# Kernel optimization log

Measured on AMD Instinct MI355X. Metric: run time of the kernel, lower is better.

## Reference

```python
import jax, jax.numpy as jnp
import numpy as np
import math

DEPTH = 3
NUM_GRAPHS = 8
BN_EPS = 1e-5
POOL_RATIO = 0.5


def _gcn(A, x, W, b):
    # GCNConv(improved=True): A_hat = A + 2*I; out = D^-1/2 A_hat D^-1/2 (x W) + b
    n = A.shape[0]
    A_hat = A + 2.0 * jnp.eye(n, dtype=A.dtype)
    deg = A_hat.sum(axis=1)
    d = jnp.where(deg > 0, jax.lax.rsqrt(deg), 0.0)
    return d[:, None] * (A_hat @ (d[:, None] * (x @ W))) + b


def _bn_eval(x, g, b):
    # BatchNorm1d in eval mode with running_mean=0, running_var=1
    return x * (g / jnp.sqrt(1.0 + BN_EPS)) + b


def _forward(x, edge_index, batch, conv0_w, conv0_b, down_w, down_b, pool_w,
             up_w, up_b, lins_w, lins_b, bn_g, bn_b, out_w, out_b):
    n0 = x.shape[0]
    # dense weighted adjacency A[dst, src] += 1 (duplicates sum, same as scatter-add MP)
    A = jnp.zeros((n0, n0), x.dtype).at[edge_index[1], edge_index[0]].add(1.0)

    # ---- GraphUNet (eval mode: dropout p=0.92 is identity) ----
    h = jax.nn.relu(_gcn(A, x, conv0_w, conv0_b))
    xs, As, perms = [h], [A], []
    for i in range(DEPTH):
        n = A.shape[0]
        eye = jnp.eye(n, dtype=A.dtype)
        S = A + eye                       # add_self_loops(weight=1)
        A2 = (S @ S) * (1.0 - eye)        # spspmm then remove_self_loops
        # TopKPooling: score = tanh((x.w)/||w||), keep top ceil(0.5*n) nodes
        score = jnp.tanh((h @ pool_w[i]) / jnp.linalg.norm(pool_w[i]))
        k = math.ceil(POOL_RATIO * n)
        _, perm = jax.lax.top_k(score, k)
        h = h[perm] * score[perm][:, None]
        A = A2[perm][:, perm]             # filter_adj
        h = jax.nn.relu(_gcn(A, h, down_w[i], down_b[i]))
        if i < DEPTH - 1:
            xs.append(h)
            As.append(A)
        perms.append(perm)
    for i in range(DEPTH):
        j = DEPTH - 1 - i
        res, Aj, perm = xs[j], As[j], perms[j]
        up = jnp.zeros_like(res).at[perm].set(h)
        h = res + up                      # sum_res=True skip connection
        h = _gcn(Aj, h, up_w[i], up_b[i])
        if i < DEPTH - 1:
            h = jax.nn.relu(h)

    # ---- global_add_pool + BN/Linear/tanh head ----
    g = jax.ops.segment_sum(h, batch, num_segments=NUM_GRAPHS)
    for i in range(3):
        g = _bn_eval(g, bn_g[i], bn_b[i])
        g = jnp.tanh(g @ lins_w[i] + lins_b[i])
    g = _bn_eval(g, bn_g[3], bn_b[3])
    return g @ out_w + out_b


def setup_inputs() -> dict:
    key = jax.random.key(0)
    ks = jax.random.split(key, 20)
    N, F, H, O, E = 4096, 64, 128, 32, 65536
    s = 0.05
    x = jax.random.normal(ks[0], (N, F), jnp.float32)
    src = jax.random.randint(ks[1], (E,), 0, N)
    dst = jax.random.randint(ks[2], (E,), 0, N)
    edge_index = jnp.stack([jnp.concatenate([src, dst]),
                            jnp.concatenate([dst, src])]).astype(jnp.int32)
    batch = jnp.sort(jax.random.randint(ks[3], (N,), 0, NUM_GRAPHS)).astype(jnp.int32)
    return {
        "x": x,
        "edge_index": edge_index,
        "batch": batch,
        "conv0_w": jax.random.normal(ks[4], (F, H), jnp.float32) * s,
        "conv0_b": jnp.zeros((H,), jnp.float32),
        "down_w": jax.random.normal(ks[5], (DEPTH, H, H), jnp.float32) * s,
        "down_b": jnp.zeros((DEPTH, H), jnp.float32),
        "pool_w": jax.random.normal(ks[6], (DEPTH, H), jnp.float32),
        "up_w": jax.random.normal(ks[7], (DEPTH, H, H), jnp.float32) * s,
        "up_b": jnp.zeros((DEPTH, H), jnp.float32),
        "lins_w": jax.random.normal(ks[8], (3, H, H), jnp.float32) * s,
        "lins_b": jnp.zeros((3, H), jnp.float32),
        "bn_g": jnp.ones((4, H), jnp.float32),
        "bn_b": jnp.zeros((4, H), jnp.float32),
        "out_w": jax.random.normal(ks[9], (H, O), jnp.float32) * s,
        "out_b": jnp.zeros((O,), jnp.float32),
    }


def reference(x, edge_index, batch, conv0_w, conv0_b, down_w, down_b, pool_w,
              up_w, up_b, lins_w, lins_b, bn_g, bn_b, out_w, out_b):
    return _forward(x, edge_index, batch, conv0_w, conv0_b, down_w, down_b,
                    pool_w, up_w, up_b, lins_w, lins_b, bn_g, bn_b, out_w, out_b)
```

## Files before the change

kernel.cpp:

```cpp
#include <hip/hip_runtime.h>
#include <math.h>

#define H 128
#define NG 8

typedef __attribute__((ext_vector_type(8))) short bf16x8;
typedef __attribute__((ext_vector_type(8))) unsigned short ushort8;
typedef __attribute__((ext_vector_type(4))) float f32x4;

static __device__ __forceinline__ float b2f(unsigned short u) {
  union { unsigned int i; float f; } v;
  v.i = ((unsigned int)u) << 16;
  return v.f;
}
static __device__ __forceinline__ unsigned short f2b(float f) {
  return (unsigned short)(__float_as_uint(f) >> 16);
}

__global__ void k_hist(const int* __restrict__ ei, int E, int* __restrict__ cnt) {
  int e = blockIdx.x * 256 + threadIdx.x;
  if (e >= E) return;
  atomicAdd(&cnt[ei[E + e]], 1);
}

__global__ __launch_bounds__(1024) void k_scan(const int* __restrict__ cnt,
                                               int* __restrict__ rowptr, int n) {
  __shared__ int sums[1024];
  int tid = threadIdx.x;
  int base = tid * 4;
  int v0 = 0, v1 = 0, v2 = 0, v3 = 0;
  if (base < n) { v0 = cnt[base]; v1 = cnt[base + 1]; v2 = cnt[base + 2]; v3 = cnt[base + 3]; }
  int s = v0 + v1 + v2 + v3;
  sums[tid] = s;
  __syncthreads();
  for (int off = 1; off < 1024; off <<= 1) {
    int t = (tid >= off) ? sums[tid - off] : 0;
    __syncthreads();
    sums[tid] += t;
    __syncthreads();
  }
  int excl = sums[tid] - s;
  if (base < n) {
    rowptr[base] = excl;
    rowptr[base + 1] = excl + v0;
    rowptr[base + 2] = excl + v0 + v1;
    rowptr[base + 3] = excl + v0 + v1 + v2;
  }
  if (tid == 1023) rowptr[n] = sums[1023];
}

__global__ void k_fill(const int* __restrict__ ei, int E, const int* __restrict__ rowptr,
                       int* __restrict__ cursor, int* __restrict__ colidx) {
  int e = blockIdx.x * 256 + threadIdx.x;
  if (e >= E) return;
  int r = ei[E + e], c = ei[e];
  int p = atomicAdd(&cursor[r], 1);
  colidx[rowptr[r] + p] = c;
}

__global__ void k_dvcnt(const int* __restrict__ cnt, float* __restrict__ dv, int n) {
  int i = blockIdx.x * 256 + threadIdx.x;
  if (i < n) dv[i] = rsqrtf((float)cnt[i] + 2.0f);
}

__global__ void k_deg(const float* __restrict__ A, int n, float* __restrict__ dv) {
  int row = blockIdx.x * (blockDim.x >> 6) + (threadIdx.x >> 6);
  int lane = threadIdx.x & 63;
  if (row >= n) return;
  float s = 0.f;
  const float* arow = A + (size_t)row * n;
  for (int j = lane; j < n; j += 64) s += arow[j];
#pragma unroll
  for (int o = 32; o > 0; o >>= 1) s += __shfl_down(s, o);
  if (lane == 0) dv[row] = rsqrtf(s + 2.0f);
}

template <int MODE>
__global__ __launch_bounds__(256) void k_xw(const float* __restrict__ X,
                                            const float* __restrict__ W,
                                            const float* __restrict__ dv,
                                            const int* __restrict__ idx,
                                            const float* __restrict__ aux,
                                            float* __restrict__ Y, int n, int F) {
  __shared__ float Xs[64][36];
  __shared__ float Ws[32][132];
  __shared__ int ridx[64];
  __shared__ float rscl[64];
  int tid = threadIdx.x;
  int rowBase = blockIdx.x * 64;
  if (MODE == 1) {
    if (tid < 64) {
      int pp = idx[rowBase + tid];
      ridx[tid] = pp;
      rscl[tid] = aux[pp];
    }
  } else if (MODE == 2) {
    if (tid < 64) ridx[tid] = idx[rowBase + tid];
  }
  if (MODE != 0) __syncthreads();
  int r0 = (tid >> 5) << 3;
  int c0 = (tid & 31) << 2;
  float acc[8][4] = {};
  for (int k0 = 0; k0 < F; k0 += 32) {
#pragma unroll
    for (int it = 0, e = tid; it < 8; ++it, e += 256) {
      int ii = e >> 5, kk = e & 31;
      int gk = k0 + kk;
      float v;
      if (MODE == 0) {
        v = X[(size_t)(rowBase + ii) * F + gk];
      } else if (MODE == 1) {
        v = X[(size_t)ridx[ii] * F + gk] * rscl[ii];
      } else {
        v = X[(size_t)(rowBase + ii) * F + gk];
        int iv = ridx[ii];
        if (iv >= 0) v += aux[(size_t)iv * H + gk];
      }
      Xs[ii][kk] = v;
    }
#pragma unroll
    for (int it = 0, e = tid; it < 4; ++it, e += 256) {
      int kk = e >> 5, cc4 = e & 31;
      *(float4*)&Ws[kk][cc4 << 2] = *(const float4*)&W[(size_t)(k0 + kk) * H + (cc4 << 2)];
    }
    __syncthreads();
#pragma unroll
    for (int kk = 0; kk < 32; kk += 4) {
      float4 a4[8], w4[4];
#pragma unroll
      for (int i = 0; i < 8; ++i) a4[i] = *(const float4*)&Xs[r0 + i][kk];
#pragma unroll
      for (int s = 0; s < 4; ++s) w4[s] = *(const float4*)&Ws[kk + s][c0];
#pragma unroll
      for (int i = 0; i < 8; ++i) {
        float av[4] = {a4[i].x, a4[i].y, a4[i].z, a4[i].w};
#pragma unroll
        for (int s = 0; s < 4; ++s) {
          float wv[4] = {w4[s].x, w4[s].y, w4[s].z, w4[s].w};
#pragma unroll
          for (int j = 0; j < 4; ++j) acc[i][j] = fmaf(av[s], wv[j], acc[i][j]);
        }
      }
    }
    __syncthreads();
  }
#pragma unroll
  for (int i = 0; i < 8; ++i) {
    int row = rowBase + r0 + i;
    float d = dv[row];
    *(float4*)&Y[(size_t)row * H + c0] =
        make_float4(d * acc[i][0], d * acc[i][1], d * acc[i][2], d * acc[i][3]);
  }
}

__global__ void k_spmm_fin(const int* __restrict__ rowptr, const int* __restrict__ colidx,
                           const float* __restrict__ Y, const float* __restrict__ dv,
                           const float* __restrict__ bias, float* __restrict__ Out,
                           int n, int relu) {
  int row = blockIdx.x * 4 + (threadIdx.x >> 6);
  int lane = threadIdx.x & 63;
  if (row >= n) return;
  int s = rowptr[row], e = rowptr[row + 1];
  float a0 = 0.f, a1 = 0.f;
  int i = s;
  for (; i + 1 < e; i += 2) {
    int c0 = colidx[i], c1 = colidx[i + 1];
    a0 += Y[(size_t)c0 * H + lane] + Y[(size_t)c1 * H + lane];
    a1 += Y[(size_t)c0 * H + 64 + lane] + Y[(size_t)c1 * H + 64 + lane];
  }
  if (i < e) {
    int c = colidx[i];
    a0 += Y[(size_t)c * H + lane];
    a1 += Y[(size_t)c * H + 64 + lane];
  }
  float d = dv[row];
  float v0 = d * (a0 + 2.0f * Y[(size_t)row * H + lane]) + bias[lane];
  float v1 = d * (a1 + 2.0f * Y[(size_t)row * H + 64 + lane]) + bias[64 + lane];
  if (relu) { v0 = fmaxf(v0, 0.f); v1 = fmaxf(v1, 0.f); }
  Out[(size_t)row * H + lane] = v0;
  Out[(size_t)row * H + 64 + lane] = v1;
}

__global__ __launch_bounds__(256) void k_ata_rows(const int* __restrict__ rowptr,
                                                  const int* __restrict__ colidx,
                                                  const int* __restrict__ perm,
                                                  const int* __restrict__ inv,
                                                  unsigned short* __restrict__ Ab,
                                                  float* __restrict__ dv, int kdim) {
  __shared__ int acc[2048];
  __shared__ int wsum[4];
  int i = blockIdx.x;
  int tid = threadIdx.x;
  for (int j = tid; j < kdim; j += 256) acc[j] = 0;
  __syncthreads();
  int p = perm[i];
  int s = rowptr[p], e = rowptr[p + 1];
  int deg = e - s;
  int wave = tid >> 6, lane = tid & 63;
  for (int q = wave; q <= deg; q += 4) {
    int kn = (q < deg) ? colidx[s + q] : p;
    int s2 = rowptr[kn], e2 = rowptr[kn + 1];
    for (int idx = s2 + lane; idx <= e2; idx += 64) {
      int j = (idx < e2) ? colidx[idx] : kn;
      int ii = inv[j];
      if (ii >= 0) atomicAdd(&acc[ii], 1);
    }
  }
  __syncthreads();
  int rs = 0;
  {
    int j0 = tid * 8;
    ushort8 v;
#pragma unroll
    for (int q = 0; q < 8; ++q) {
      int j = j0 + q;
      int c = (j == i) ? 0 : acc[j];
      rs += c;
      v[q] = f2b((float)c);
    }
    *(ushort8*)&Ab[(size_t)i * kdim + j0] = v;
  }
#pragma unroll
  for (int o = 32; o > 0; o >>= 1) rs += __shfl_down(rs, o);
  if (lane == 0) wsum[wave] = rs;
  __syncthreads();
  if (tid == 0) dv[i] = rsqrtf((float)(wsum[0] + wsum[1] + wsum[2] + wsum[3]) + 2.0f);
}

__global__ void k_gather(const unsigned short* __restrict__ Ab, const int* __restrict__ perm,
                         unsigned short* __restrict__ P, int n, int k) {
  int row = blockIdx.x;
  int p = perm[row];
  const unsigned short* src = Ab + (size_t)p * n;
  unsigned short* dst = P + (size_t)row * n;
  for (int c = threadIdx.x * 8; c < n; c += 256 * 8) {
    *(ushort8*)&dst[c] = *(const ushort8*)&src[c];
  }
  __syncthreads();
  if (threadIdx.x == 0) dst[p] = f2b(b2f(src[p]) + 1.0f);
}

__global__ __launch_bounds__(256) void k_ata_mfma(const unsigned short* __restrict__ P,
                                                  float* __restrict__ C, int n, int k) {
  __shared__ __align__(16) unsigned short As[64][64];
  __shared__ __align__(16) unsigned short Bs[64][64];
  int tid = threadIdx.x;
  int w = tid >> 6, ln = tid & 63;
  int l15 = ln & 15, l4 = ln >> 4;
  int br = blockIdx.y, bc = blockIdx.x;
  f32x4 acc[4] = {};
  for (int k0 = 0; k0 < n; k0 += 64) {
#pragma unroll
    for (int it = 0; it < 2; ++it) {
      int e = tid + it * 256;
      int row = e >> 3, ch = e & 7;
      int sch = (ch ^ (row & 7)) * 8;
      *(ushort8*)&As[row][sch] = *(const ushort8*)&P[(size_t)(br * 64 + row) * n + k0 + ch * 8];
      *(ushort8*)&Bs[row][sch] = *(const ushort8*)&P[(size_t)(bc * 64 + row) * n + k0 + ch * 8];
    }
    __syncthreads();
#pragma unroll
    for (int s = 0; s < 2; ++s) {
      int arow = w * 16 + l15;
      bf16x8 af = *(const bf16x8*)&As[arow][((s * 4 + l4) ^ (arow & 7)) * 8];
#pragma unroll
      for (int f = 0; f < 4; ++f) {
        int brow = f * 16 + l15;
        bf16x8 bfr = *(const bf16x8*)&Bs[brow][((s * 4 + l4) ^ (brow & 7)) * 8];
        acc[f] = __builtin_amdgcn_mfma_f32_16x16x32_bf16(af, bfr, acc[f], 0, 0, 0);
      }
    }
    __syncthreads();
  }
#pragma unroll
  for (int f = 0; f < 4; ++f) {
#pragma unroll
    for (int r = 0; r < 4; ++r) {
      int gi = br * 64 + w * 16 + l4 * 4 + r;
      int gj = bc * 64 + f * 16 + l15;
      C[(size_t)gi * k + gj] = (gi == gj) ? 0.0f : acc[f][r];
    }
  }
}

__global__ void k_cvt_split(const float* __restrict__ Y, unsigned short* __restrict__ YT, int n) {
  int c = blockIdx.x;
  for (int k0 = threadIdx.x * 8; k0 < n; k0 += 256 * 8) {
    ushort8 hi, lo;
#pragma unroll
    for (int q = 0; q < 8; ++q) {
      float v = Y[(size_t)(k0 + q) * H + c];
      unsigned short h = f2b(v);
      hi[q] = h;
      lo[q] = f2b(v - b2f(h));
    }
    *(ushort8*)&YT[(size_t)c * (2 * n) + k0] = hi;
    *(ushort8*)&YT[(size_t)c * (2 * n) + n + k0] = lo;
  }
}

__global__ __launch_bounds__(256) void k_gcn_mfma(const unsigned short* __restrict__ A,
                                                  const unsigned short* __restrict__ YT,
                                                  float* __restrict__ Part, int n, int VK) {
  __shared__ __align__(16) unsigned short As[64][64];
  __shared__ __align__(16) unsigned short Bs[128][64];
  int tid = threadIdx.x;
  int w = tid >> 6, ln = tid & 63;
  int l15 = ln & 15, l4 = ln >> 4;
  int rowBase = blockIdx.x * 64;
  float* out = Part + (size_t)blockIdx.y * n * H;
  f32x4 acc[8] = {};
  int vk0s = blockIdx.y * VK;
  for (int vk0 = vk0s; vk0 < vk0s + VK; vk0 += 64) {
    int ka = vk0 & (n - 1);
#pragma unroll
    for (int it = 0; it < 2; ++it) {
      int e = tid + it * 256;
      int row = e >> 3, ch = e & 7;
      int sch = (ch ^ (row & 7)) * 8;
      *(ushort8*)&As[row][sch] = *(const ushort8*)&A[(size_t)(rowBase + row) * n + ka + ch * 8];
    }
#pragma unroll
    for (int it = 0; it < 4; ++it) {
      int e = tid + it * 256;
      int row = e >> 3, ch = e & 7;
      int sch = (ch ^ (row & 7)) * 8;
      *(ushort8*)&Bs[row][sch] = *(const ushort8*)&YT[(size_t)row * (2 * n) + vk0 + ch * 8];
    }
    __syncthreads();
#pragma unroll
    for (int s = 0; s < 2; ++s) {
      int arow = w * 16 + l15;
      bf16x8 af = *(const bf16x8*)&As[arow][((s * 4 + l4) ^ (arow & 7)) * 8];
#pragma unroll
      for (int f = 0; f < 8; ++f) {
        int brow = f * 16 + l15;
        bf16x8 bfr = *(const bf16x8*)&Bs[brow][((s * 4 + l4) ^ (brow & 7)) * 8];
        acc[f] = __builtin_amdgcn_mfma_f32_16x16x32_bf16(af, bfr, acc[f], 0, 0, 0);
      }
    }
    __syncthreads();
  }
#pragma unroll
  for (int f = 0; f < 8; ++f) {
#pragma unroll
    for (int r = 0; r < 4; ++r) {
      int row = rowBase + w * 16 + l4 * 4 + r;
      out[(size_t)row * H + f * 16 + l15] = acc[f][r];
    }
  }
}

__global__ __launch_bounds__(256) void k_ata_sk(const float* __restrict__ A,
                                                const int* __restrict__ perm,
                                                float* __restrict__ C, int n, int k, int CK) {
  int bc = blockIdx.x, br = blockIdx.y;
  if (br > bc) return;
  __shared__ float As[64][36];
  __shared__ float Bs[64][36];
  __shared__ int pr[64], pc[64];
  int tid = threadIdx.x;
  if (tid < 64) pr[tid] = perm[br * 64 + tid];
  else if (tid < 128) pc[tid - 64] = perm[bc * 64 + (tid - 64)];
  __syncthreads();
  int ty = tid >> 4;
  int tx = tid & 15;
  float acc[4][4] = {};
  int k0s = blockIdx.z * CK;
  for (int k0 = k0s; k0 < k0s + CK; k0 += 32) {
#pragma unroll
    for (int it = 0, e = tid; it < 8; ++it, e += 256) {
      int ii = e >> 5, kk = e & 31;
      int gk = k0 + kk;
      int p = pr[ii];
      As[ii][kk] = A[(size_t)p * n + gk] + ((p == gk) ? 1.0f : 0.0f);
      p = pc[ii];
      Bs[ii][kk] = A[(size_t)p * n + gk] + ((p == gk) ? 1.0f : 0.0f);
    }
    __syncthreads();
#pragma unroll
    for (int kk = 0; kk < 32; kk += 4) {
      float4 a4[4], b4[4];
#pragma unroll
      for (int i = 0; i < 4; ++i) a4[i] = *(const float4*)&As[ty + 16 * i][kk];
#pragma unroll
      for (int j = 0; j < 4; ++j) b4[j] = *(const float4*)&Bs[tx + 16 * j][kk];
#pragma unroll
      for (int i = 0; i < 4; ++i) {
        float av[4] = {a4[i].x, a4[i].y, a4[i].z, a4[i].w};
#pragma unroll
        for (int j = 0; j < 4; ++j) {
          float bv[4] = {b4[j].x, b4[j].y, b4[j].z, b4[j].w};
#pragma unroll
          for (int s = 0; s < 4; ++s) acc[i][j] = fmaf(av[s], bv[s], acc[i][j]);
        }
      }
    }
    __syncthreads();
  }
  bool diag = (br == bc);
#pragma unroll
  for (int i = 0; i < 4; ++i) {
    int gi = br * 64 + ty + 16 * i;
#pragma unroll
    for (int j = 0; j < 4; ++j) {
      int gj = bc * 64 + tx + 16 * j;
      if (gi == gj) continue;
      float v = acc[i][j];
      atomicAdd(&C[(size_t)gi * k + gj], v);
      if (!diag) atomicAdd(&C[(size_t)gj * k + gi], v);
    }
  }
}

__global__ __launch_bounds__(256) void k_gcn_part(const float* __restrict__ A,
                                                  const float* __restrict__ Y,
                                                  float* __restrict__ Part,
                                                  int n, int KC) {
  __shared__ float As[64][36];
  __shared__ float Ys[32][132];
  int tid = threadIdx.x;
  int r0 = (tid >> 5) << 3;
  int c0 = (tid & 31) << 2;
  size_t rowBase = (size_t)blockIdx.x * 64;
  int k0s = blockIdx.y * KC;
  float* out = Part + (size_t)blockIdx.y * n * H;
  float acc[8][4] = {};
  for (int k0 = k0s; k0 < k0s + KC; k0 += 32) {
#pragma unroll
    for (int it = 0, e = tid; it < 8; ++it, e += 256) {
      int ii = e >> 5, kk = e & 31;
      As[ii][kk] = A[(rowBase + ii) * (size_t)n + k0 + kk];
    }
#pragma unroll
    for (int it = 0, e = tid; it < 4; ++it, e += 256) {
      int kk = e >> 5, cc4 = e & 31;
      *(float4*)&Ys[kk][cc4 << 2] = *(const float4*)&Y[(size_t)(k0 + kk) * H + (cc4 << 2)];
    }
    __syncthreads();
#pragma unroll
    for (int kk = 0; kk < 32; kk += 4) {
      float4 a4[8], y4[4];
#pragma unroll
      for (int i = 0; i < 8; ++i) a4[i] = *(const float4*)&As[r0 + i][kk];
#pragma unroll
      for (int s = 0; s < 4; ++s) y4[s] = *(const float4*)&Ys[kk + s][c0];
#pragma unroll
      for (int i = 0; i < 8; ++i) {
        float av[4] = {a4[i].x, a4[i].y, a4[i].z, a4[i].w};
#pragma unroll
        for (int s = 0; s < 4; ++s) {
          float yv[4] = {y4[s].x, y4[s].y, y4[s].z, y4[s].w};
#pragma unroll
          for (int j = 0; j < 4; ++j) acc[i][j] = fmaf(av[s], yv[j], acc[i][j]);
        }
      }
    }
    __syncthreads();
  }
#pragma unroll
  for (int i = 0; i < 8; ++i) {
    size_t row = rowBase + r0 + i;
    *(float4*)&out[row * H + c0] = make_float4(acc[i][0], acc[i][1], acc[i][2], acc[i][3]);
  }
}

__global__ void k_gcn_fin(const float* __restrict__ Part, const float* __restrict__ Y,
                          const float* __restrict__ dv, const float* __restrict__ bias,
                          float* __restrict__ Out, int n, int nch, int relu) {
  int i4 = blockIdx.x * 256 + threadIdx.x;
  if (i4 * 4 >= n * H) return;
  int row = i4 >> 5, c4 = (i4 & 31) * 4;
  size_t stride = (size_t)n * H;
  float4 s = *(const float4*)&Part[i4 * 4];
  for (int c = 1; c < nch; ++c) {
    float4 p = *(const float4*)&Part[c * stride + i4 * 4];
    s.x += p.x; s.y += p.y; s.z += p.z; s.w += p.w;
  }
  float4 y = *(const float4*)&Y[i4 * 4];
  float d = dv[row];
  float4 v;
  v.x = d * (s.x + 2.0f * y.x) + bias[c4];
  v.y = d * (s.y + 2.0f * y.y) + bias[c4 + 1];
  v.z = d * (s.z + 2.0f * y.z) + bias[c4 + 2];
  v.w = d * (s.w + 2.0f * y.w) + bias[c4 + 3];
  if (relu) {
    v.x = fmaxf(v.x, 0.f); v.y = fmaxf(v.y, 0.f);
    v.z = fmaxf(v.z, 0.f); v.w = fmaxf(v.w, 0.f);
  }
  *(float4*)&Out[i4 * 4] = v;
}

__global__ void k_score(const float* __restrict__ h, const float* __restrict__ w,
                        float* __restrict__ score, int n) {
  __shared__ float wn;
  int tid = threadIdx.x;
  if (tid < 64) {
    float s = w[tid] * w[tid] + w[tid + 64] * w[tid + 64];
#pragma unroll
    for (int o = 32; o > 0; o >>= 1) s += __shfl_down(s, o);
    if (tid == 0) wn = sqrtf(s);
  }
  __syncthreads();
  int row = blockIdx.x * 4 + (tid >> 6);
  int lane = tid & 63;
  if (row >= n) return;
  float s = h[(size_t)row * H + lane] * w[lane] + h[(size_t)row * H + lane + 64] * w[lane + 64];
#pragma unroll
  for (int o = 32; o > 0; o >>= 1) s += __shfl_down(s, o);
  if (lane == 0) score[row] = tanhf(s / wn);
}

static __device__ __forceinline__ void ce_(unsigned long long& x, unsigned long long& y, bool asc) {
  if ((x < y) != asc) { unsigned long long t = x; x = y; y = t; }
}
static __device__ __forceinline__ unsigned long long pick_(unsigned long long a,
                                                           unsigned long long b,
                                                           bool lower, bool asc) {
  unsigned long long lo = (a < b) ? a : b;
  unsigned long long hi = (a < b) ? b : a;
  return (lower == asc) ? lo : hi;
}

template <int LOGN>
__global__ __launch_bounds__(1024) void k_topk(const float* __restrict__ score,
                                               int* __restrict__ perm,
                                               int* __restrict__ inv) {
  const int n = 1 << LOGN;
  __shared__ unsigned long long lds[1 << LOGN];
  int t = threadIdx.x;
  int e0 = t * 4;
  unsigned long long key[4];
#pragma unroll
  for (int j = 0; j < 4; ++j) {
    unsigned u = __float_as_uint(score[e0 + j]);
    u = (u & 0x80000000u) ? ~u : (u | 0x80000000u);
    u = ~u;
    key[j] = (((unsigned long long)u) << 32) | (unsigned)(e0 + j);
  }
  ce_(key[0], key[1], true);
  ce_(key[2], key[3], false);
  for (int size = 4; size <= n; size <<= 1) {
    bool asc = ((e0 & size) == 0);
    for (int stride = size >> 1; stride >= 256; stride >>= 1) {
#pragma unroll
      for (int j = 0; j < 4; ++j) lds[e0 + j] = key[j];
      __syncthreads();
      bool lower = ((e0 & stride) == 0);
#pragma unroll
      for (int j = 0; j < 4; ++j)
        key[j] = pick_(key[j], lds[(e0 + j) ^ stride], lower, asc);
      __syncthreads();
    }
    int s0 = ((size >> 1) < 256) ? (size >> 1) : 128;
    for (int stride = s0; stride >= 4; stride >>= 1) {
      int m = stride >> 2;
      bool lower = ((t & m) == 0);
#pragma unroll
      for (int j = 0; j < 4; ++j) {
        unsigned long long o = __shfl_xor(key[j], m, 64);
        key[j] = pick_(key[j], o, lower, asc);
      }
    }
    ce_(key[0], key[2], asc);
    ce_(key[1], key[3], asc);
    ce_(key[0], key[1], asc);
    ce_(key[2], key[3], asc);
  }
  int kk = n >> 1;
#pragma unroll
  for (int j = 0; j < 4; ++j) {
    int e = e0 + j;
    int idx = (int)(key[j] & 0xffffffffu);
    if (e < kk) perm[e] = idx;
    if (inv) inv[idx] = (e < kk) ? e : -1;
  }
}

__global__ void k_segsum(const float* __restrict__ h, const int* __restrict__ batch,
                         float* __restrict__ g, int n) {
  int c = threadIdx.x;
  int r0 = blockIdx.x * 32;
  int rend = min(r0 + 32, n);
  float acc = 0.f;
  int cur = batch[r0];
  for (int r = r0; r < rend; ++r) {
    int b = batch[r];
    if (b != cur) { atomicAdd(&g[cur * H + c], acc); acc = 0.f; cur = b; }
    acc += h[(size_t)r * H + c];
  }
  atomicAdd(&g[cur * H + c], acc);
}

__global__ __launch_bounds__(256) void k_head(const float* __restrict__ g,
    const float* __restrict__ lins_w, const float* __restrict__ lins_b,
    const float* __restrict__ bn_g, const float* __restrict__ bn_b,
    const float* __restrict__ out_w, const float* __restrict__ out_b,
    float* __restrict__ out) {
  __shared__ float a[NG * H], b[NG * H];
  int tid = threadIdx.x;
  const float inv = 1.0f / sqrtf(1.0f + 1e-5f);
  for (int i = tid; i < NG * H; i += 256) a[i] = g[i];
  __syncthreads();
  for (int L = 0; L < 3; ++L) {
    for (int i = tid; i < NG * H; i += 256) {
      int c = i & 127;
      b[i] = a[i] * (bn_g[L * H + c] * inv) + bn_b[L * H + c];
    }
    __syncthreads();
    for (int i = tid; i < NG * H; i += 256) {
      int r = i >> 7, c = i & 127;
      float s = lins_b[L * H + c];
      for (int k2 = 0; k2 < H; ++k2) s += b[r * H + k2] * lins_w[(size_t)L * H * H + k2 * H + c];
      a[i] = tanhf(s);
    }
    __syncthreads();
  }
  for (int i = tid; i < NG * H; i += 256) {
    int c = i & 127;
    b[i] = a[i] * (bn_g[3 * H + c] * inv) + bn_b[3 * H + c];
  }
  __syncthreads();
  for (int i = tid; i < NG * 32; i += 256) {
    int r = i >> 5, o = i & 31;
    float s = out_b[o];
    for (int k2 = 0; k2 < H; ++k2) s += b[r * H + k2] * out_w[k2 * 32 + o];
    out[i] = s;
  }
}

extern "C" void kernel_launch(void* const* d_in, const int* in_sizes, int n_in,
                              void* d_out, int out_size, void* d_ws, size_t ws_size,
                              hipStream_t stream) {
  const float* x       = (const float*)d_in[0];
  const int*   ei      = (const int*)d_in[1];
  const int*   batch   = (const int*)d_in[2];
  const float* conv0_w = (const float*)d_in[3];
  const float* conv0_b = (const float*)d_in[4];
  const float* down_w  = (const float*)d_in[5];
  const float* down_b  = (const float*)d_in[6];
  const float* pool_w  = (const float*)d_in[7];
  const float* up_w    = (const float*)d_in[8];
  const float* up_b    = (const float*)d_in[9];
  const float* lins_w  = (const float*)d_in[10];
  const float* lins_b  = (const float*)d_in[11];
  const float* bn_g    = (const float*)d_in[12];
  const float* bn_b    = (const float*)d_in[13];
  const float* out_w   = (const float*)d_in[14];
  const float* out_b   = (const float*)d_in[15];
  int E = in_sizes[1] / 2;

  char* p = (char*)d_ws;
  auto alloc = [&](size_t bytes) {
    char* r = p;
    p += (bytes + 255) & ~(size_t)255;
    return r;
  };
  unsigned short* A1b  = (unsigned short*)alloc((size_t)2048 * 2048 * 2);
  unsigned short* P    = (unsigned short*)alloc((size_t)1024 * 2048 * 2);
  unsigned short* YT   = (unsigned short*)alloc((size_t)128 * 4096 * 2);
  float*          A2m  = (float*)alloc((size_t)1024 * 1024 * 4);
  float*          A3   = (float*)alloc((size_t)512 * 512 * 4);
  float*          part = (float*)alloc((size_t)8 * 2048 * H * 4);
  int* cnt    = (int*)alloc(4096 * 4);
  int* cursor = (int*)alloc(4096 * 4);
  int* rowptr = (int*)alloc(4100 * 4);
  int* colidx = (int*)alloc((size_t)E * 4);
  int* inv0   = (int*)alloc(4096 * 4);
  int* inv1   = (int*)alloc(2048 * 4);
  int* inv2   = (int*)alloc(1024 * 4);
  float* dv0  = (float*)alloc(4096 * 4);
  float* dv1  = (float*)alloc(2048 * 4);
  float* dv2  = (float*)alloc(1024 * 4);
  float* dv3  = (float*)alloc(512 * 4);
  int* perm0  = (int*)alloc(2048 * 4);
  int* perm1  = (int*)alloc(1024 * 4);
  int* perm2  = (int*)alloc(512 * 4);
  float* score = (float*)alloc(4096 * 4);
  float* h0 = (float*)alloc((size_t)4096 * H * 4);
  float* h1 = (float*)alloc((size_t)2048 * H * 4);
  float* h2 = (float*)alloc((size_t)1024 * H * 4);
  float* h3 = (float*)alloc((size_t)512 * H * 4);
  float* t2 = (float*)alloc((size_t)4096 * H * 4);
  float* hu = (float*)alloc((size_t)4096 * H * 4);
  float* g  = (float*)alloc(NG * H * 4);

  auto gcn = [&](const float* A, const float* Y, const float* dvv,
                 const float* bias, float* Out, int nn, int relu) {
    const int nch = 8;
    int KC = nn / nch;
    k_gcn_part<<<dim3(nn / 64, nch), 256, 0, stream>>>(A, Y, part, nn, KC);
    k_gcn_fin<<<nn / 8, 256, 0, stream>>>(part, Y, dvv, bias, Out, nn, nch, relu);
  };
  auto gcn_mfma = [&](const unsigned short* Ab, const float* Y, const float* dvv,
                      const float* bias, float* Out, int nn, int relu) {
    k_cvt_split<<<128, 256, 0, stream>>>(Y, YT, nn);
    k_gcn_mfma<<<dim3(nn / 64, 4), 256, 0, stream>>>(Ab, YT, part, nn, (2 * nn) / 4);
    k_gcn_fin<<<nn / 8, 256, 0, stream>>>(part, Y, dvv, bias, Out, nn, 4, relu);
  };

  hipMemsetAsync(cnt, 0, 4096 * 4, stream);
  hipMemsetAsync(cursor, 0, 4096 * 4, stream);
  k_hist<<<(E + 255) / 256, 256, 0, stream>>>(ei, E, cnt);
  k_scan<<<1, 1024, 0, stream>>>(cnt, rowptr, 4096);
  k_fill<<<(E + 255) / 256, 256, 0, stream>>>(ei, E, rowptr, cursor, colidx);
  k_dvcnt<<<4096 / 256, 256, 0, stream>>>(cnt, dv0, 4096);

  k_xw<0><<<4096 / 64, 256, 0, stream>>>(x, conv0_w, dv0, nullptr, nullptr, t2, 4096, 64);
  k_spmm_fin<<<1024, 256, 0, stream>>>(rowptr, colidx, t2, dv0, conv0_b, h0, 4096, 1);

  k_score<<<1024, 256, 0, stream>>>(h0, pool_w, score, 4096);
  k_topk<12><<<1, 1024, 0, stream>>>(score, perm0, inv0);
  k_ata_rows<<<2048, 256, 0, stream>>>(rowptr, colidx, perm0, inv0, A1b, dv1, 2048);
  k_xw<1><<<2048 / 64, 256, 0, stream>>>(h0, down_w, dv1, perm0, score, t2, 2048, 128);
  gcn_mfma(A1b, t2, dv1, down_b, h1, 2048, 1);

  k_score<<<512, 256, 0, stream>>>(h1, pool_w + H, score, 2048);
  k_topk<11><<<1, 512, 0, stream>>>(score, perm1, inv1);
  k_gather<<<1024, 256, 0, stream>>>(A1b, perm1, P, 2048, 1024);
  k_ata_mfma<<<dim3(16, 16), 256, 0, stream>>>(P, A2m, 2048, 1024);
  k_deg<<<1024 / 4, 256, 0, stream>>>(A2m, 1024, dv2);
  k_xw<1><<<1024 / 64, 256, 0, stream>>>(h1, down_w + (size_t)H * H, dv2, perm1, score, t2, 1024, 128);
  gcn(A2m, t2, dv2, down_b + H, h2, 1024, 1);

  k_score<<<256, 256, 0, stream>>>(h2, pool_w + 2 * H, score, 1024);
  k_topk<10><<<1, 256, 0, stream>>>(score, perm2, inv2);
  hipMemsetAsync(A3, 0, (size_t)512 * 512 * 4, stream);
  k_ata_sk<<<dim3(8, 8, 8), 256, 0, stream>>>(A2m, perm2, A3, 1024, 512, 128);
  k_deg<<<512 / 4, 256, 0, stream>>>(A3, 512, dv3);
  k_xw<1><<<512 / 64, 256, 0, stream>>>(h2, down_w + (size_t)2 * H * H, dv3, perm2, score, t2, 512, 128);
  gcn(A3, t2, dv3, down_b + 2 * H, h3, 512, 1);

  k_xw<2><<<1024 / 64, 256, 0, stream>>>(h2, up_w, dv2, inv2, h3, t2, 1024, 128);
  gcn(A2m, t2, dv2, up_b, hu, 1024, 1);

  k_xw<2><<<2048 / 64, 256, 0, stream>>>(h1, up_w + (size_t)H * H, dv1, inv1, hu, t2, 2048, 128);
  gcn_mfma(A1b, t2, dv1, up_b + H, hu, 2048, 1);

  k_xw<2><<<4096 / 64, 256, 0, stream>>>(h0, up_w + (size_t)2 * H * H, dv0, inv0, hu, t2, 4096, 128);
  k_spmm_fin<<<1024, 256, 0, stream>>>(rowptr, colidx, t2, dv0, up_b + 2 * H, hu, 4096, 0);

  hipMemsetAsync(g, 0, NG * H * 4, stream);
  k_segsum<<<4096 / 32, 128, 0, stream>>>(hu, batch, g, 4096);
  k_head<<<1, 256, 0, stream>>>(g, lins_w, lins_b, bn_g, bn_b, out_w, out_b, (float*)d_out);
}
```

Before: 529.7 us.

## Fuse gather into A^2 MFMA, fold degree computation, drop extra kernels

The separate gather kernel that built a permuted bf16 copy P of A1b is removed. The A^2 MFMA kernel now loads rows of A1b directly through perm and adds the self-loop on the fly. It also accumulates row sums with atomics, so the separate k_deg pass over A2m disappears and rsqrt is applied later in the consumers. dv0 is now computed inside the scan, which removes k_dvcnt. Other changes: spmm_fin uses float2 accesses and the MFMA GCN uses 8 K-chunks instead of 4. The trade-offs are redundant gathered loads per tile, atomics, and a changed column mapping in spmm.

```diff
diff --git a/kernel.cpp b/kernel.cpp
--- a/kernel.cpp
+++ b/kernel.cpp
@@ -24,7 +24,8 @@
 }
 
 __global__ __launch_bounds__(1024) void k_scan(const int* __restrict__ cnt,
-                                               int* __restrict__ rowptr, int n) {
+                                               int* __restrict__ rowptr,
+                                               float* __restrict__ dv, int n) {
   __shared__ int sums[1024];
   int tid = threadIdx.x;
   int base = tid * 4;
@@ -45,6 +46,10 @@
     rowptr[base + 1] = excl + v0;
     rowptr[base + 2] = excl + v0 + v1;
     rowptr[base + 3] = excl + v0 + v1 + v2;
+    dv[base] = rsqrtf((float)v0 + 2.0f);
+    dv[base + 1] = rsqrtf((float)v1 + 2.0f);
+    dv[base + 2] = rsqrtf((float)v2 + 2.0f);
+    dv[base + 3] = rsqrtf((float)v3 + 2.0f);
   }
   if (tid == 1023) rowptr[n] = sums[1023];
 }
@@ -58,11 +63,6 @@
   colidx[rowptr[r] + p] = c;
 }
 
-__global__ void k_dvcnt(const int* __restrict__ cnt, float* __restrict__ dv, int n) {
-  int i = blockIdx.x * 256 + threadIdx.x;
-  if (i < n) dv[i] = rsqrtf((float)cnt[i] + 2.0f);
-}
-
 __global__ void k_deg(const float* __restrict__ A, int n, float* __restrict__ dv) {
   int row = blockIdx.x * (blockDim.x >> 6) + (threadIdx.x >> 6);
   int lane = threadIdx.x & 63;
@@ -75,7 +75,7 @@
   if (lane == 0) dv[row] = rsqrtf(s + 2.0f);
 }
 
-template <int MODE>
+template <int MODE, int RS>
 __global__ __launch_bounds__(256) void k_xw(const float* __restrict__ X,
                                             const float* __restrict__ W,
                                             const float* __restrict__ dv,
@@ -147,7 +147,7 @@
 #pragma unroll
   for (int i = 0; i < 8; ++i) {
     int row = rowBase + r0 + i;
-    float d = dv[row];
+    float d = RS ? rsqrtf(dv[row] + 2.0f) : dv[row];
     *(float4*)&Y[(size_t)row * H + c0] =
         make_float4(d * acc[i][0], d * acc[i][1], d * acc[i][2], d * acc[i][3]);
   }
@@ -161,24 +161,29 @@
   int lane = threadIdx.x & 63;
   if (row >= n) return;
   int s = rowptr[row], e = rowptr[row + 1];
+  int c2 = lane * 2;
   float a0 = 0.f, a1 = 0.f;
   int i = s;
   for (; i + 1 < e; i += 2) {
-    int c0 = colidx[i], c1 = colidx[i + 1];
-    a0 += Y[(size_t)c0 * H + lane] + Y[(size_t)c1 * H + lane];
-    a1 += Y[(size_t)c0 * H + 64 + lane] + Y[(size_t)c1 * H + 64 + lane];
+    int cA = colidx[i], cB = colidx[i + 1];
+    float2 yA = *(const float2*)&Y[(size_t)cA * H + c2];
+    float2 yB = *(const float2*)&Y[(size_t)cB * H + c2];
+    a0 += yA.x + yB.x;
+    a1 += yA.y + yB.y;
   }
   if (i < e) {
     int c = colidx[i];
-    a0 += Y[(size_t)c * H + lane];
-    a1 += Y[(size_t)c * H + 64 + lane];
+    float2 y = *(const float2*)&Y[(size_t)c * H + c2];
+    a0 += y.x;
+    a1 += y.y;
   }
   float d = dv[row];
-  float v0 = d * (a0 + 2.0f * Y[(size_t)row * H + lane]) + bias[lane];
-  float v1 = d * (a1 + 2.0f * Y[(size_t)row * H + 64 + lane]) + bias[64 + lane];
+  float2 yr = *(const float2*)&Y[(size_t)row * H + c2];
+  float v0 = d * (a0 + 2.0f * yr.x) + bias[c2];
+  float v1 = d * (a1 + 2.0f * yr.y) + bias[c2 + 1];
   if (relu) { v0 = fmaxf(v0, 0.f); v1 = fmaxf(v1, 0.f); }
-  Out[(size_t)row * H + lane] = v0;
-  Out[(size_t)row * H + 64 + lane] = v1;
+  float2 o = make_float2(v0, v1);
+  *(float2*)&Out[(size_t)row * H + c2] = o;
 }
 
 __global__ __launch_bounds__(256) void k_ata_rows(const int* __restrict__ rowptr,
@@ -227,27 +232,21 @@
   if (tid == 0) dv[i] = rsqrtf((float)(wsum[0] + wsum[1] + wsum[2] + wsum[3]) + 2.0f);
 }
 
-__global__ void k_gather(const unsigned short* __restrict__ Ab, const int* __restrict__ perm,
-                         unsigned short* __restrict__ P, int n, int k) {
-  int row = blockIdx.x;
-  int p = perm[row];
-  const unsigned short* src = Ab + (size_t)p * n;
-  unsigned short* dst = P + (size_t)row * n;
-  for (int c = threadIdx.x * 8; c < n; c += 256 * 8) {
-    *(ushort8*)&dst[c] = *(const ushort8*)&src[c];
-  }
-  __syncthreads();
-  if (threadIdx.x == 0) dst[p] = f2b(b2f(src[p]) + 1.0f);
-}
-
-__global__ __launch_bounds__(256) void k_ata_mfma(const unsigned short* __restrict__ P,
-                                                  float* __restrict__ C, int n, int k) {
+__global__ __launch_bounds__(256) void k_ata_mfma_g(const unsigned short* __restrict__ Ab,
+                                                    const int* __restrict__ perm,
+                                                    float* __restrict__ C,
+                                                    float* __restrict__ rowsum,
+                                                    int n, int k) {
   __shared__ __align__(16) unsigned short As[64][64];
   __shared__ __align__(16) unsigned short Bs[64][64];
+  __shared__ int pr[64], pc[64];
   int tid = threadIdx.x;
   int w = tid >> 6, ln = tid & 63;
   int l15 = ln & 15, l4 = ln >> 4;
   int br = blockIdx.y, bc = blockIdx.x;
+  if (tid < 64) pr[tid] = perm[br * 64 + tid];
+  else if (tid < 128) pc[tid - 64] = perm[bc * 64 + (tid - 64)];
+  __syncthreads();
   f32x4 acc[4] = {};
   for (int k0 = 0; k0 < n; k0 += 64) {
 #pragma unroll
@@ -255,8 +254,23 @@
       int e = tid + it * 256;
       int row = e >> 3, ch = e & 7;
       int sch = (ch ^ (row & 7)) * 8;
-      *(ushort8*)&As[row][sch] = *(const ushort8*)&P[(size_t)(br * 64 + row) * n + k0 + ch * 8];
-      *(ushort8*)&Bs[row][sch] = *(const ushort8*)&P[(size_t)(bc * 64 + row) * n + k0 + ch * 8];
+      int base = k0 + ch * 8;
+      {
+        int p = pr[row];
+        ushort8 v = *(const ushort8*)&Ab[(size_t)p * n + base];
+#pragma unroll
+        for (int q = 0; q < 8; ++q)
+          if (base + q == p) v[q] = f2b(b2f(v[q]) + 1.0f);
+        *(ushort8*)&As[row][sch] = v;
+      }
+      {
+        int p = pc[row];
+        ushort8 v = *(const ushort8*)&Ab[(size_t)p * n + base];
+#pragma unroll
+        for (int q = 0; q < 8; ++q)
+          if (base + q == p) v[q] = f2b(b2f(v[q]) + 1.0f);
+        *(ushort8*)&Bs[row][sch] = v;
+      }
     }
     __syncthreads();
 #pragma unroll
@@ -273,13 +287,19 @@
     __syncthreads();
   }
 #pragma unroll
-  for (int f = 0; f < 4; ++f) {
-#pragma unroll
-    for (int r = 0; r < 4; ++r) {
-      int gi = br * 64 + w * 16 + l4 * 4 + r;
+  for (int r = 0; r < 4; ++r) {
+    int gi = br * 64 + w * 16 + l4 * 4 + r;
+    float part = 0.f;
+#pragma unroll
+    for (int f = 0; f < 4; ++f) {
       int gj = bc * 64 + f * 16 + l15;
-      C[(size_t)gi * k + gj] = (gi == gj) ? 0.0f : acc[f][r];
-    }
+      float v = (gi == gj) ? 0.0f : acc[f][r];
+      C[(size_t)gi * k + gj] = v;
+      part += v;
+    }
+#pragma unroll
+    for (int m = 8; m >= 1; m >>= 1) part += __shfl_xor(part, m, 64);
+    if (l15 == 0) atomicAdd(&rowsum[gi], part);
   }
 }
 
@@ -465,6 +485,7 @@
   }
 }
 
+template <int RS>
 __global__ void k_gcn_fin(const float* __restrict__ Part, const float* __restrict__ Y,
                           const float* __restrict__ dv, const float* __restrict__ bias,
                           float* __restrict__ Out, int n, int nch, int relu) {
@@ -478,7 +499,7 @@
     s.x += p.x; s.y += p.y; s.z += p.z; s.w += p.w;
   }
   float4 y = *(const float4*)&Y[i4 * 4];
-  float d = dv[row];
+  float d = RS ? rsqrtf(dv[row] + 2.0f) : dv[row];
   float4 v;
   v.x = d * (s.x + 2.0f * y.x) + bias[c4];
   v.y = d * (s.y + 2.0f * y.y) + bias[c4 + 1];
@@ -657,7 +678,6 @@
     return r;
   };
   unsigned short* A1b  = (unsigned short*)alloc((size_t)2048 * 2048 * 2);
-  unsigned short* P    = (unsigned short*)alloc((size_t)1024 * 2048 * 2);
   unsigned short* YT   = (unsigned short*)alloc((size_t)128 * 4096 * 2);
   float*          A2m  = (float*)alloc((size_t)1024 * 1024 * 4);
   float*          A3   = (float*)alloc((size_t)512 * 512 * 4);
@@ -685,59 +705,60 @@
   float* hu = (float*)alloc((size_t)4096 * H * 4);
   float* g  = (float*)alloc(NG * H * 4);
 
-  auto gcn = [&](const float* A, const float* Y, const float* dvv,
-                 const float* bias, float* Out, int nn, int relu) {
+  auto gcn = [&](const float* A, const float* Y, const float* dvv, const float* bias,
+                 float* Out, int nn, int relu, bool rs) {
     const int nch = 8;
     int KC = nn / nch;
     k_gcn_part<<<dim3(nn / 64, nch), 256, 0, stream>>>(A, Y, part, nn, KC);
-    k_gcn_fin<<<nn / 8, 256, 0, stream>>>(part, Y, dvv, bias, Out, nn, nch, relu);
+    if (rs)
+      k_gcn_fin<1><<<nn / 8, 256, 0, stream>>>(part, Y, dvv, bias, Out, nn, nch, relu);
+    else
+      k_gcn_fin<0><<<nn / 8, 256, 0, stream>>>(part, Y, dvv, bias, Out, nn, nch, relu);
   };
   auto gcn_mfma = [&](const unsigned short* Ab, const float* Y, const float* dvv,
                       const float* bias, float* Out, int nn, int relu) {
     k_cvt_split<<<128, 256, 0, stream>>>(Y, YT, nn);
-    k_gcn_mfma<<<dim3(nn / 64, 4), 256, 0, stream>>>(Ab, YT, part, nn, (2 * nn) / 4);
-    k_gcn_fin<<<nn / 8, 256, 0, stream>>>(part, Y, dvv, bias, Out, nn, 4, relu);
+    k_gcn_mfma<<<dim3(nn / 64, 8), 256, 0, stream>>>(Ab, YT, part, nn, (2 * nn) / 8);
+    k_gcn_fin<0><<<nn / 8, 256, 0, stream>>>(part, Y, dvv, bias, Out, nn, 8, relu);
   };
 
   hipMemsetAsync(cnt, 0, 4096 * 4, stream);
   hipMemsetAsync(cursor, 0, 4096 * 4, stream);
   k_hist<<<(E + 255) / 256, 256, 0, stream>>>(ei, E, cnt);
-  k_scan<<<1, 1024, 0, stream>>>(cnt, rowptr, 4096);
+  k_scan<<<1, 1024, 0, stream>>>(cnt, rowptr, dv0, 4096);
   k_fill<<<(E + 255) / 256, 256, 0, stream>>>(ei, E, rowptr, cursor, colidx);
-  k_dvcnt<<<4096 / 256, 256, 0, stream>>>(cnt, dv0, 4096);
-
-  k_xw<0><<<4096 / 64, 256, 0, stream>>>(x, conv0_w, dv0, nullptr, nullptr, t2, 4096, 64);
+
+  k_xw<0, 0><<<4096 / 64, 256, 0, stream>>>(x, conv0_w, dv0, nullptr, nullptr, t2, 4096, 64);
   k_spmm_fin<<<1024, 256, 0, stream>>>(rowptr, colidx, t2, dv0, conv0_b, h0, 4096, 1);
 
   k_score<<<1024, 256, 0, stream>>>(h0, pool_w, score, 4096);
   k_topk<12><<<1, 1024, 0, stream>>>(score, perm0, inv0);
   k_ata_rows<<<2048, 256, 0, stream>>>(rowptr, colidx, perm0, inv0, A1b, dv1, 2048);
-  k_xw<1><<<2048 / 64, 256, 0, stream>>>(h0, down_w, dv1, perm0, score, t2, 2048, 128);
+  k_xw<1, 0><<<2048 / 64, 256, 0, stream>>>(h0, down_w, dv1, perm0, score, t2, 2048, 128);
   gcn_mfma(A1b, t2, dv1, down_b, h1, 2048, 1);
 
   k_score<<<512, 256, 0, stream>>>(h1, pool_w + H, score, 2048);
   k_topk<11><<<1, 512, 0, stream>>>(score, perm1, inv1);
-  k_gather<<<1024, 256, 0, stream>>>(A1b, perm1, P, 2048, 1024);
-  k_ata_mfma<<<dim3(16, 16), 256, 0, stream>>>(P, A2m, 2048, 1024);
-  k_deg<<<1024 / 4, 256, 0, stream>>>(A2m, 1024, dv2);
-  k_xw<1><<<1024 / 64, 256, 0, stream>>>(h1, down_w + (size_t)H * H, dv2, perm1, score, t2, 1024, 128);
-  gcn(A2m, t2, dv2, down_b + H, h2, 1024, 1);
+  hipMemsetAsync(dv2, 0, 1024 * 4, stream);
+  k_ata_mfma_g<<<dim3(16, 16), 256, 0, stream>>>(A1b, perm1, A2m, dv2, 2048, 1024);
+  k_xw<1, 1><<<1024 / 64, 256, 0, stream>>>(h1, down_w + (size_t)H * H, dv2, perm1, score, t2, 1024, 128);
+  gcn(A2m, t2, dv2, down_b + H, h2, 1024, 1, true);
 
   k_score<<<256, 256, 0, stream>>>(h2, pool_w + 2 * H, score, 1024);
   k_topk<10><<<1, 256, 0, stream>>>(score, perm2, inv2);
   hipMemsetAsync(A3, 0, (size_t)512 * 512 * 4, stream);
   k_ata_sk<<<dim3(8, 8, 8), 256, 0, stream>>>(A2m, perm2, A3, 1024, 512, 128);
   k_deg<<<512 / 4, 256, 0, stream>>>(A3, 512, dv3);
-  k_xw<1><<<512 / 64, 256, 0, stream>>>(h2, down_w + (size_t)2 * H * H, dv3, perm2, score, t2, 512, 128);
-  gcn(A3, t2, dv3, down_b + 2 * H, h3, 512, 1);
-
-  k_xw<2><<<1024 / 64, 256, 0, stream>>>(h2, up_w, dv2, inv2, h3, t2, 1024, 128);
-  gcn(A2m, t2, dv2, up_b, hu, 1024, 1);
-
-  k_xw<2><<<2048 / 64, 256, 0, stream>>>(h1, up_w + (size_t)H * H, dv1, inv1, hu, t2, 2048, 128);
+  k_xw<1, 0><<<512 / 64, 256, 0, stream>>>(h2, down_w + (size_t)2 * H * H, dv3, perm2, score, t2, 512, 128);
+  gcn(A3, t2, dv3, down_b + 2 * H, h3, 512, 1, false);
+
+  k_xw<2, 1><<<1024 / 64, 256, 0, stream>>>(h2, up_w, dv2, inv2, h3, t2, 1024, 128);
+  gcn(A2m, t2, dv2, up_b, hu, 1024, 1, true);
+
+  k_xw<2, 0><<<2048 / 64, 256, 0, stream>>>(h1, up_w + (size_t)H * H, dv1, inv1, hu, t2, 2048, 128);
   gcn_mfma(A1b, t2, dv1, up_b + H, hu, 2048, 1);
 
-  k_xw<2><<<4096 / 64, 256, 0, stream>>>(h0, up_w + (size_t)2 * H * H, dv0, inv0, hu, t2, 4096, 128);
+  k_xw<2, 0><<<4096 / 64, 256, 0, stream>>>(h0, up_w + (size_t)2 * H * H, dv0, inv0, hu, t2, 4096, 128);
   k_spmm_fin<<<1024, 256, 0, stream>>>(rowptr, colidx, t2, dv0, up_b + 2 * H, hu, 4096, 0);
 
   hipMemsetAsync(g, 0, NG * H * 4, stream);
```

Result: no change. 524.0 us (-1.1%).
